# Kernel tuning notes

Measured on AMD Instinct MI355X. Metric: run time of the kernel, lower is better.

The kernel has to match this reference:

```python
import math
import jax, jax.numpy as jnp
import numpy as np

DIM = 2048
HID = 4 * DIM
SEQ = 2048
BATCH = 2
EPS = 1e-5


def _layernorm(x, g, b):
    mu = jnp.mean(x, axis=-1, keepdims=True)
    var = jnp.var(x, axis=-1, keepdims=True)
    return (x - mu) * jax.lax.rsqrt(var + EPS) * g + b


def setup_inputs() -> dict:
    key = jax.random.key(0)
    ks = jax.random.split(key, 12)
    s = 1.0 / math.sqrt(DIM)
    x = jax.random.normal(ks[0], (BATCH, SEQ, DIM), dtype=jnp.float32)
    # additive causal mask: 0 on/below diagonal, -1e9 above
    mask = jnp.where(jnp.tril(jnp.ones((SEQ, SEQ), dtype=bool)), 0.0, -1e9).astype(jnp.float32)
    freqs_cis = jax.random.normal(ks[1], (SEQ, 64), dtype=jnp.float32)  # unused by forward
    return {
        "x": x,
        "mask": mask,
        "start_pos": 0,
        "freqs_cis": freqs_cis,
        "wq": jax.random.normal(ks[2], (DIM, DIM), dtype=jnp.float32) * s,
        "bq": jnp.zeros((DIM,), dtype=jnp.float32),
        "wk": jax.random.normal(ks[3], (DIM, DIM), dtype=jnp.float32) * s,
        "bk": jnp.zeros((DIM,), dtype=jnp.float32),
        "wv": jax.random.normal(ks[4], (DIM, DIM), dtype=jnp.float32) * s,
        "bv": jnp.zeros((DIM,), dtype=jnp.float32),
        "g_ln1": jnp.ones((DIM,), dtype=jnp.float32),
        "b_ln1": jnp.zeros((DIM,), dtype=jnp.float32),
        "g_ln2": jnp.ones((DIM,), dtype=jnp.float32),
        "b_ln2": jnp.zeros((DIM,), dtype=jnp.float32),
        "w1": jax.random.normal(ks[5], (DIM, HID), dtype=jnp.float32) * s,
        "b1": jnp.zeros((HID,), dtype=jnp.float32),
        "w2": jax.random.normal(ks[6], (HID, DIM), dtype=jnp.float32) * (1.0 / math.sqrt(HID)),
        "b2": jnp.zeros((DIM,), dtype=jnp.float32),
    }


def reference(x, mask, start_pos, freqs_cis, wq, bq, wk, bk, wv, bv,
              g_ln1, b_ln1, g_ln2, b_ln2, w1, b1, w2, b2):
    # pre-norm attention (no head split; scale by sqrt(full dim); dropout=eval identity)
    h = _layernorm(x, g_ln1, b_ln1)
    q = h @ wq + bq
    k = h @ wk + bk
    v = h @ wv + bv
    scores = jnp.einsum('bqd,bkd->bqk', q, k) / math.sqrt(DIM) + mask
    attn = jax.nn.softmax(scores, axis=-1)
    attn_out = jnp.einsum('bqk,bkd->bqd', attn, v)
    h2 = _layernorm(x + attn_out, g_ln2, b_ln2)
    ffn = jax.nn.gelu(h2 @ w1 + b1, approximate=False) @ w2 + b2
    # NOTE: original code adds FFN output to the ORIGINAL x (attn residual dropped here)
    return x + ffn
```

## Files before the change

### kernel.cpp

```cpp
#include <hip/hip_runtime.h>
#include <math.h>

#define DIM_ 2048
#define HID_ 8192
#define SEQ_ 2048
#define BATCH_ 2
#define TOK_ (BATCH_*SEQ_)

typedef __attribute__((ext_vector_type(4))) float f32x4;
typedef __attribute__((ext_vector_type(8))) __bf16 bf16x8;
typedef __attribute__((ext_vector_type(4))) unsigned int u32x4;
typedef __attribute__((ext_vector_type(4))) short s16x4;
typedef __attribute__((ext_vector_type(8))) short s16x8;
typedef __attribute__((address_space(3))) short* lds_sp;

__device__ __forceinline__ short f2bf(float f) {
  union { float f; unsigned u; } v; v.f = f;
  unsigned r = v.u + 0x7FFFu + ((v.u >> 16) & 1u);
  return (short)(r >> 16);
}
__device__ __forceinline__ float bf2f(short s) {
  union { unsigned u; float f; } v; v.u = ((unsigned)(unsigned short)s) << 16;
  return v.f;
}

__device__ __forceinline__ f32x4 mfma16(u32x4 a, u32x4 b, f32x4 c) {
  return __builtin_amdgcn_mfma_f32_16x16x32_bf16(
      __builtin_bit_cast(bf16x8, a), __builtin_bit_cast(bf16x8, b), c, 0, 0, 0);
}

#define DSR(dst, addr) asm volatile("ds_read_b128 %0, %1" : "=v"(dst) : "v"(addr))
#define BARv()  __builtin_amdgcn_s_barrier()
#define LGKMW(n) do { asm volatile("s_waitcnt lgkmcnt(" #n ")" ::: "memory"); \
                      __builtin_amdgcn_sched_barrier(0); } while(0)
#define VM3()   asm volatile("s_waitcnt vmcnt(3)" ::: "memory")
#define VM4()   asm volatile("s_waitcnt vmcnt(4)" ::: "memory")
#define PRIO1() __builtin_amdgcn_s_setprio(1)
#define PRIO0() __builtin_amdgcn_s_setprio(0)

#define TILE_MAP(BM, BN) \
  const int nwg  = gridDim.x * gridDim.y; \
  const int orig = blockIdx.y * gridDim.x + blockIdx.x; \
  const int wgid = (orig & 7) * (nwg >> 3) + (orig >> 3); \
  const int gy4  = (int)gridDim.y << 2; \
  const int rem  = wgid % gy4; \
  const int tn   = ((wgid / gy4) * 4 + (rem & 3)) * (BN); \
  const int tm   = (rem >> 2) * (BM);

template<int EPI>
__device__ __forceinline__ void epi_store(void* Cv, const float* bias, const float* aux,
                                          int z, long long sC, int ldc, int N,
                                          int row, int col, float v)
{
  if (EPI == 1) {
    ((float*)Cv + (long long)z * sC)[(long long)row * ldc + col] = v;
  } else if (EPI == 0) {
    v += bias[col];
    ((short*)Cv + (long long)z * sC)[(long long)row * ldc + col] = f2bf(v);
  } else if (EPI == 2) {
    v += bias[col];
    v = 0.5f * v * (1.0f + erff(v * 0.70710678118654752f));
    ((short*)Cv + (long long)z * sC)[(long long)row * ldc + col] = f2bf(v);
  } else if (EPI == 3) {
    v += bias[col] + aux[(long long)row * ldc + col];
    ((float*)Cv + (long long)z * sC)[(long long)row * ldc + col] = v;
  } else {
    v = v * 0.022097086912079608f + aux[(long long)row * ldc + col];
    ((short*)Cv + (long long)z * sC)[(long long)row * ldc + col] = f2bf(v);
  }
}

#define G256_RD1(slot) do { \
  const unsigned s_ = (unsigned)(slot)*16384u; \
  DSR(af[0], aRd + s_);          DSR(af[1], aRd + s_ + 1024u); \
  DSR(af[2], aRd + s_ + 2048u);  DSR(af[3], aRd + s_ + 3072u); \
  DSR(af[4], aRd + s_ + 4096u);  DSR(af[5], aRd + s_ + 5120u); \
  DSR(af[6], aRd + s_ + 6144u);  DSR(af[7], aRd + s_ + 7168u); \
  DSR(bf0[0], bRd + s_);         DSR(bf0[1], bRd + s_ + 1024u); \
} while(0)

#define G256_RD2(slot) do { \
  const unsigned s_ = (unsigned)(slot)*16384u; \
  DSR(bf1[0], bRd + s_ + 2048u); DSR(bf1[1], bRd + s_ + 3072u); \
} while(0)

#define G256_MM(c0, bA, bB) do { \
  _Pragma("unroll") \
  for (int fr_ = 0; fr_ < 8; ++fr_) { \
    acc[fr_][(c0)]   = mfma16(af[fr_], bA, acc[fr_][(c0)]); \
    acc[fr_][(c0)+1] = mfma16(af[fr_], bB, acc[fr_][(c0)+1]); \
  } \
} while(0)

template<int EPI>
__global__ __launch_bounds__(512, 2)
void gemm256(const short* __restrict__ A, const short* __restrict__ B,
             void* __restrict__ Cv, const float* __restrict__ bias,
             const float* __restrict__ aux,
             int M, int N, int K, int lda, int ldb, int ldc,
             long long sA, long long sB, long long sC)
{
  __shared__ __align__(16) short As[3*256*32];
  __shared__ __align__(16) short Bs[3*256*32];
  const int lane = threadIdx.x & 63;
  const int wave = threadIdx.x >> 6;
  const int wr = wave >> 2, wc = wave & 3;
  TILE_MAP(256, 256)
  const int z = blockIdx.z;
  A += (long long)z * sA;
  B += (long long)z * sB;

  const int NT = K >> 5;

  const int rr   = wave * 16 + (lane >> 2);
  const int soff = (((lane & 3) ^ ((lane >> 3) & 3)) << 3);
  const short* pA = A + (long long)(tm + rr) * lda + soff;
  const short* pB = B + (long long)(tn + rr) * ldb + soff;
  const long long lda128 = 128LL * lda;
  const long long ldb128 = 128LL * ldb;

  auto stA = [&](int t, int slot) {
    const long long ko = (long long)t << 5;
    __builtin_amdgcn_global_load_lds(
        (const __attribute__((address_space(1))) void*)(pA + ko),
        (__attribute__((address_space(3))) void*)(As + slot * 8192 + wave * 512), 16, 0, 0);
    __builtin_amdgcn_global_load_lds(
        (const __attribute__((address_space(1))) void*)(pA + lda128 + ko),
        (__attribute__((address_space(3))) void*)(As + slot * 8192 + 4096 + wave * 512), 16, 0, 0);
  };
  auto stB = [&](int t, int slot) {
    const long long ko = (long long)t << 5;
    __builtin_amdgcn_global_load_lds(
        (const __attribute__((address_space(1))) void*)(pB + ko),
        (__attribute__((address_space(3))) void*)(Bs + slot * 8192 + wave * 512), 16, 0, 0);
    __builtin_amdgcn_global_load_lds(
        (const __attribute__((address_space(1))) void*)(pB + ldb128 + ko),
        (__attribute__((address_space(3))) void*)(Bs + slot * 8192 + 4096 + wave * 512), 16, 0, 0);
  };

  const unsigned asB = (unsigned)(unsigned long long)(lds_sp)As;
  const unsigned bsB = (unsigned)(unsigned long long)(lds_sp)Bs;
  const int l15 = lane & 15, l4 = lane >> 4;
  const unsigned offk = (unsigned)((l4 ^ ((l15 >> 1) & 3)) << 4);
  const unsigned aRd = asB + (unsigned)((wr * 128 + l15) * 64) + offk;
  const unsigned bRd = bsB + (unsigned)((wc * 64 + l15) * 64) + offk;

  f32x4 acc[8][4] = {};
  u32x4 af[8], bf0[2], bf1[2];

  stA(0, 0); stB(0, 0);
  stA(1 < NT ? 1 : 0, 1); stB(1 < NT ? 1 : 0, 1);
  VM4();
  BARv();

  int rd = 0;
  #pragma unroll 1
  for (int t = 0; t < NT; ++t) {
    const int st = rd + 2 >= 3 ? rd - 1 : rd + 2;
    const int tc = t + 2 < NT ? t + 2 : NT - 1;
    G256_RD1(rd);
    G256_RD2(rd);
    stA(tc, st); stB(tc, st);
    LGKMW(2);
    PRIO1(); G256_MM(0, bf0[0], bf0[1]);
    LGKMW(0);
    G256_MM(2, bf1[0], bf1[1]); PRIO0();
    VM4();
    BARv();
    rd = rd + 1 >= 3 ? 0 : rd + 1;
  }

  const int row0 = tm + wr * 128 + l4 * 4;
  const int col0 = tn + wc * 64 + l15;
  #pragma unroll
  for (int fr = 0; fr < 8; ++fr)
    #pragma unroll
    for (int j = 0; j < 4; ++j)
      #pragma unroll
      for (int fc = 0; fc < 4; ++fc)
        epi_store<EPI>(Cv, bias, aux, z, sC, ldc, N,
                       row0 + fr * 16 + j, col0 + fc * 16, acc[fr][fc][j]);
}

#define HRD2(slot) do { \
  const unsigned a_ = aBaseH + (unsigned)(slot)*8192u; \
  const unsigned b_ = bBaseH + (unsigned)(slot)*16384u; \
  DSR(bf[0], b_ + offk);          DSR(bf[1], b_ + 1024u + offk); \
  DSR(bf[2], b_ + 2048u + offk);  DSR(bf[3], b_ + 3072u + offk); \
  DSR(af[0], a_ + offk);          DSR(af[1], a_ + 1024u + offk); \
  DSR(af[2], a_ + 2048u + offk);  DSR(af[3], a_ + 3072u + offk); \
} while(0)

#define HROW(mi) do { \
  _Pragma("unroll") \
  for (int ni = 0; ni < 4; ++ni) \
    acc[mi][ni] = mfma16(af[mi], bf[ni], acc[mi][ni]); \
} while(0)

template<int EPI>
__global__ __launch_bounds__(512, 4)
void gemm_hi(const short* __restrict__ A, const short* __restrict__ B,
             void* __restrict__ Cv, const float* __restrict__ bias,
             const float* __restrict__ aux,
             int M, int N, int K, int lda, int ldb, int ldc,
             long long sA, long long sB, long long sC)
{
  __shared__ __align__(16) short As[3*128*32];
  __shared__ __align__(16) short Bs[3*256*32];
  const int lane = threadIdx.x & 63;
  const int wave = threadIdx.x >> 6;
  const int wr = wave >> 2, wc = wave & 3;
  TILE_MAP(128, 256)
  const int z = blockIdx.z;
  A += (long long)z * sA;
  B += (long long)z * sB;

  const int NT = K >> 5;

  const int rr   = wave * 16 + (lane >> 2);
  const int soff = (((lane & 3) ^ ((lane >> 3) & 3)) << 3);
  const short* pA = A + (long long)(tm + rr) * lda + soff;
  const short* pB = B + (long long)(tn + rr) * ldb + soff;
  const long long ldb128 = 128LL * ldb;

  auto stage = [&](int t, int slot) {
    const long long ko = (long long)t << 5;
    __builtin_amdgcn_global_load_lds(
        (const __attribute__((address_space(1))) void*)(pA + ko),
        (__attribute__((address_space(3))) void*)(As + slot * 4096 + wave * 512), 16, 0, 0);
    __builtin_amdgcn_global_load_lds(
        (const __attribute__((address_space(1))) void*)(pB + ko),
        (__attribute__((address_space(3))) void*)(Bs + slot * 8192 + wave * 512), 16, 0, 0);
    __builtin_amdgcn_global_load_lds(
        (const __attribute__((address_space(1))) void*)(pB + ldb128 + ko),
        (__attribute__((address_space(3))) void*)(Bs + slot * 8192 + 4096 + wave * 512), 16, 0, 0);
  };

  const unsigned asB = (unsigned)(unsigned long long)(lds_sp)As;
  const unsigned bsB = (unsigned)(unsigned long long)(lds_sp)Bs;
  const int l15 = lane & 15, l4 = lane >> 4;
  const unsigned offk  = (unsigned)((l4 ^ ((l15 >> 1) & 3)) << 4);
  const unsigned aBaseH = asB + (unsigned)(wr * 4096 + l15 * 64);
  const unsigned bBaseH = bsB + (unsigned)(wc * 4096 + l15 * 64);

  f32x4 acc[4][4] = {};
  u32x4 af[4], bf[4];

  stage(0, 0);
  stage(1 < NT ? 1 : 0, 1);
  VM3();
  BARv();

  int rd = 0;
  #pragma unroll 1
  for (int t = 0; t < NT; ++t) {
    const int st = rd + 2 >= 3 ? rd - 1 : rd + 2;
    const int tc = t + 2 < NT ? t + 2 : NT - 1;
    HRD2(rd);
    stage(tc, st);
    LGKMW(3);
    PRIO1(); HROW(0);
    LGKMW(2); HROW(1);
    LGKMW(1); HROW(2);
    LGKMW(0); HROW(3); PRIO0();
    VM3();
    BARv();
    rd = rd + 1 >= 3 ? 0 : rd + 1;
  }

  const int row0 = tm + wr * 64 + l4 * 4;
  const int col0 = tn + wc * 64 + l15;
  #pragma unroll
  for (int mi = 0; mi < 4; ++mi)
    #pragma unroll
    for (int j = 0; j < 4; ++j)
      #pragma unroll
      for (int ni = 0; ni < 4; ++ni)
        epi_store<EPI>(Cv, bias, aux, z, sC, ldc, N,
                       row0 + mi * 16 + j, col0 + ni * 16, acc[mi][ni][j]);
}

__global__ __launch_bounds__(256)
void ln_kernel(const float* __restrict__ x, const float* __restrict__ res,
               const float* __restrict__ g, const float* __restrict__ b,
               short* __restrict__ out, int hasres)
{
  const int row = blockIdx.x;
  const int tid = threadIdx.x;
  const float4* X = (const float4*)x + (long long)row * 512;
  float4 v0 = X[tid], v1 = X[tid + 256];
  if (hasres) {
    const float4* R = (const float4*)res + (long long)row * 512;
    float4 r0 = R[tid], r1 = R[tid + 256];
    v0.x += r0.x; v0.y += r0.y; v0.z += r0.z; v0.w += r0.w;
    v1.x += r1.x; v1.y += r1.y; v1.z += r1.z; v1.w += r1.w;
  }
  float s1 = v0.x + v0.y + v0.z + v0.w + v1.x + v1.y + v1.z + v1.w;
  float s2 = v0.x*v0.x + v0.y*v0.y + v0.z*v0.z + v0.w*v0.w
           + v1.x*v1.x + v1.y*v1.y + v1.z*v1.z + v1.w*v1.w;
  #pragma unroll
  for (int o = 32; o > 0; o >>= 1) { s1 += __shfl_xor(s1, o); s2 += __shfl_xor(s2, o); }
  __shared__ float red[8];
  if ((tid & 63) == 0) { red[tid >> 6] = s1; red[4 + (tid >> 6)] = s2; }
  __syncthreads();
  s1 = red[0] + red[1] + red[2] + red[3];
  s2 = red[4] + red[5] + red[6] + red[7];
  const float mean = s1 * (1.0f / 2048.0f);
  const float var  = s2 * (1.0f / 2048.0f) - mean * mean;
  const float rstd = rsqrtf(var + 1e-5f);
  const float4* G  = (const float4*)g;
  const float4* Bb = (const float4*)b;
  float4 g0 = G[tid], g1 = G[tid + 256], b0 = Bb[tid], b1 = Bb[tid + 256];
  s16x4 o0, o1;
  o0[0] = f2bf((v0.x - mean) * rstd * g0.x + b0.x);
  o0[1] = f2bf((v0.y - mean) * rstd * g0.y + b0.y);
  o0[2] = f2bf((v0.z - mean) * rstd * g0.z + b0.z);
  o0[3] = f2bf((v0.w - mean) * rstd * g0.w + b0.w);
  o1[0] = f2bf((v1.x - mean) * rstd * g1.x + b1.x);
  o1[1] = f2bf((v1.y - mean) * rstd * g1.y + b1.y);
  o1[2] = f2bf((v1.z - mean) * rstd * g1.z + b1.z);
  o1[3] = f2bf((v1.w - mean) * rstd * g1.w + b1.w);
  *(s16x4*)&out[(long long)row * 2048 + tid * 4]        = o0;
  *(s16x4*)&out[(long long)row * 2048 + 1024 + tid * 4] = o1;
}

__global__ __launch_bounds__(256)
void softmax_bf16_kernel(short* __restrict__ probs)
{
  const long long row = blockIdx.x;
  const int tid = threadIdx.x;
  short* P = probs + row * 2048 + tid * 8;
  s16x8 in = *(const s16x8*)P;
  float a[8];
  #pragma unroll
  for (int i = 0; i < 8; ++i) a[i] = bf2f(in[i]);
  float mx = a[0];
  #pragma unroll
  for (int i = 1; i < 8; ++i) mx = fmaxf(mx, a[i]);
  #pragma unroll
  for (int o = 32; o > 0; o >>= 1) mx = fmaxf(mx, __shfl_xor(mx, o));
  __shared__ float red[8];
  if ((tid & 63) == 0) red[tid >> 6] = mx;
  __syncthreads();
  mx = fmaxf(fmaxf(red[0], red[1]), fmaxf(red[2], red[3]));
  float e[8], sum = 0.f;
  #pragma unroll
  for (int i = 0; i < 8; ++i) { e[i] = __expf(a[i] - mx); sum += e[i]; }
  #pragma unroll
  for (int o = 32; o > 0; o >>= 1) sum += __shfl_xor(sum, o);
  if ((tid & 63) == 0) red[4 + (tid >> 6)] = sum;
  __syncthreads();
  sum = red[4] + red[5] + red[6] + red[7];
  const float inv = 1.0f / sum;
  s16x8 o;
  #pragma unroll
  for (int i = 0; i < 8; ++i) o[i] = f2bf(e[i] * inv);
  *(s16x8*)P = o;
}

__global__ __launch_bounds__(256)
void cvt_transpose64(const float* __restrict__ in, short* __restrict__ out,
                     int R, int C)
{
  __shared__ float t[64][69];
  const int r0 = blockIdx.y << 6, c0 = blockIdx.x << 6;
  const int tx = threadIdx.x & 15, ty = threadIdx.x >> 4;
  #pragma unroll
  for (int p = 0; p < 4; ++p) {
    const int r = ty + p * 16;
    float4 v = *(const float4*)&in[(long long)(r0 + r) * C + c0 + tx * 4];
    t[r][tx*4+0] = v.x; t[r][tx*4+1] = v.y; t[r][tx*4+2] = v.z; t[r][tx*4+3] = v.w;
  }
  __syncthreads();
  #pragma unroll
  for (int p = 0; p < 4; ++p) {
    const int oc = ty + p * 16;
    s16x4 o;
    o[0] = f2bf(t[tx*4+0][oc]); o[1] = f2bf(t[tx*4+1][oc]);
    o[2] = f2bf(t[tx*4+2][oc]); o[3] = f2bf(t[tx*4+3][oc]);
    *(s16x4*)&out[(long long)(c0 + oc) * R + r0 + tx * 4] = o;
  }
}

__global__ __launch_bounds__(256)
void transpose_bf16_kernel(const short* __restrict__ in, short* __restrict__ out,
                           int ldin, int ldout, long long sin_, long long sout_)
{
  __shared__ short t[32][33];
  in  += (long long)blockIdx.z * sin_;
  out += (long long)blockIdx.z * sout_;
  const int tx = threadIdx.x & 31, ty = threadIdx.x >> 5;
  const int r0 = blockIdx.y << 5, c0 = blockIdx.x << 5;
  #pragma unroll
  for (int i = 0; i < 32; i += 8)
    t[ty + i][tx] = in[(long long)(r0 + ty + i) * ldin + c0 + tx];
  __syncthreads();
  #pragma unroll
  for (int i = 0; i < 32; i += 8)
    out[(long long)(c0 + ty + i) * ldout + r0 + tx] = t[tx][ty + i];
}

__global__ __launch_bounds__(256)
void concat_bias_kernel(const float* a, const float* b, const float* c, float* o)
{
  const int i = blockIdx.x * 256 + threadIdx.x;
  o[i] = i < 2048 ? a[i] : (i < 4096 ? b[i - 2048] : c[i - 4096]);
}

extern "C" void kernel_launch(void* const* d_in, const int* in_sizes, int n_in,
                              void* d_out, int out_size, void* d_ws, size_t ws_size,
                              hipStream_t stream)
{
  const float* x    = (const float*)d_in[0];
  const float* mask = (const float*)d_in[1];
  const float* wq   = (const float*)d_in[4];
  const float* bq   = (const float*)d_in[5];
  const float* wk   = (const float*)d_in[6];
  const float* bk   = (const float*)d_in[7];
  const float* wv   = (const float*)d_in[8];
  const float* bv   = (const float*)d_in[9];
  const float* g1   = (const float*)d_in[10];
  const float* b1   = (const float*)d_in[11];
  const float* g2   = (const float*)d_in[12];
  const float* b2   = (const float*)d_in[13];
  const float* w1   = (const float*)d_in[14];
  const float* bw1  = (const float*)d_in[15];
  const float* w2   = (const float*)d_in[16];
  const float* bw2  = (const float*)d_in[17];
  float* out = (float*)d_out;

  char* p = (char*)d_ws;
  auto take = [&](size_t bytes) { char* r = p; p += (bytes + 255) & ~(size_t)255; return r; };
  short* wqkvT = (short*)take((size_t)3 * DIM_ * DIM_ * 2);
  short* w1T   = (short*)take((size_t)DIM_ * HID_ * 2);
  short* w2T   = (short*)take((size_t)HID_ * DIM_ * 2);
  short* h_bf  = (short*)take((size_t)TOK_ * DIM_ * 2);
  short* qkv   = (short*)take((size_t)TOK_ * 3 * DIM_ * 2);
  short* vT    = (short*)take((size_t)BATCH_ * DIM_ * SEQ_ * 2);
  float* attno = (float*)take((size_t)TOK_ * DIM_ * 4);
  short* attn  = (short*)take((size_t)BATCH_ * SEQ_ * SEQ_ * 2);
  float* cbias = (float*)take((size_t)3 * DIM_ * 4);
  short* ffn1  = qkv;
  short* h2    = h_bf;

  const dim3 blk(256), gblk(512);
  cvt_transpose64<<<dim3(DIM_/64, DIM_/64), blk, 0, stream>>>(wq, wqkvT, DIM_, DIM_);
  cvt_transpose64<<<dim3(DIM_/64, DIM_/64), blk, 0, stream>>>(wk, wqkvT + (size_t)DIM_*DIM_, DIM_, DIM_);
  cvt_transpose64<<<dim3(DIM_/64, DIM_/64), blk, 0, stream>>>(wv, wqkvT + (size_t)2*DIM_*DIM_, DIM_, DIM_);
  cvt_transpose64<<<dim3(HID_/64, DIM_/64), blk, 0, stream>>>(w1, w1T, DIM_, HID_);
  cvt_transpose64<<<dim3(DIM_/64, HID_/64), blk, 0, stream>>>(w2, w2T, HID_, DIM_);
  concat_bias_kernel<<<24, blk, 0, stream>>>(bq, bk, bv, cbias);
  ln_kernel<<<TOK_, blk, 0, stream>>>(x, nullptr, g1, b1, h_bf, 0);
  gemm256<0><<<dim3(6144/256, TOK_/256, 1), gblk, 0, stream>>>(
      h_bf, wqkvT, qkv, cbias, nullptr, TOK_, 6144, DIM_, DIM_, DIM_, 6144, 0, 0, 0);
  gemm_hi<4><<<dim3(SEQ_/256, SEQ_/128, BATCH_), gblk, 0, stream>>>(
      qkv, qkv + DIM_, attn, nullptr, mask, SEQ_, SEQ_, DIM_, 6144, 6144, SEQ_,
      (long long)SEQ_ * 6144, (long long)SEQ_ * 6144, (long long)SEQ_ * SEQ_);
  softmax_bf16_kernel<<<BATCH_ * SEQ_, blk, 0, stream>>>(attn);
  transpose_bf16_kernel<<<dim3(DIM_/32, SEQ_/32, BATCH_), blk, 0, stream>>>(
      qkv + 2*DIM_, vT, 6144, SEQ_, (long long)SEQ_ * 6144, (long long)DIM_ * SEQ_);
  gemm_hi<1><<<dim3(DIM_/256, SEQ_/128, BATCH_), gblk, 0, stream>>>(
      attn, vT, attno, nullptr, nullptr, SEQ_, DIM_, SEQ_, SEQ_, SEQ_, DIM_,
      (long long)SEQ_ * SEQ_, (long long)DIM_ * SEQ_, (long long)SEQ_ * DIM_);
  ln_kernel<<<TOK_, blk, 0, stream>>>(x, attno, g2, b2, h2, 1);
  gemm256<2><<<dim3(HID_/256, TOK_/256, 1), gblk, 0, stream>>>(
      h2, w1T, ffn1, bw1, nullptr, TOK_, HID_, DIM_, DIM_, DIM_, HID_, 0, 0, 0);
  gemm_hi<3><<<dim3(DIM_/256, TOK_/128, 1), gblk, 0, stream>>>(
      ffn1, w2T, out, bw2, x, TOK_, DIM_, HID_, HID_, HID_, DIM_, 0, 0, 0);
}
```

Measured before the change: 625.2 us.

## Replace 256x256 GEMM main loop with 8-phase ping-pong schedule using K=64 tiles

```diff
diff --git a/kernel.cpp b/kernel.cpp
--- a/kernel.cpp
+++ b/kernel.cpp
@@ -37,6 +37,8 @@
 #define VM4()   asm volatile("s_waitcnt vmcnt(4)" ::: "memory")
 #define PRIO1() __builtin_amdgcn_s_setprio(1)
 #define PRIO0() __builtin_amdgcn_s_setprio(0)
+#define AS1 const __attribute__((address_space(1))) void*
+#define AS3 __attribute__((address_space(3))) void*
 
 #define TILE_MAP(BM, BN) \
   const int nwg  = gridDim.x * gridDim.y; \
@@ -70,38 +72,43 @@
   }
 }
 
-#define G256_RD1(slot) do { \
-  const unsigned s_ = (unsigned)(slot)*16384u; \
-  DSR(af[0], aRd + s_);          DSR(af[1], aRd + s_ + 1024u); \
-  DSR(af[2], aRd + s_ + 2048u);  DSR(af[3], aRd + s_ + 3072u); \
-  DSR(af[4], aRd + s_ + 4096u);  DSR(af[5], aRd + s_ + 5120u); \
-  DSR(af[6], aRd + s_ + 6144u);  DSR(af[7], aRd + s_ + 7168u); \
-  DSR(bf0[0], bRd + s_);         DSR(bf0[1], bRd + s_ + 1024u); \
-} while(0)
-
-#define G256_RD2(slot) do { \
-  const unsigned s_ = (unsigned)(slot)*16384u; \
-  DSR(bf1[0], bRd + s_ + 2048u); DSR(bf1[1], bRd + s_ + 3072u); \
-} while(0)
-
-#define G256_MM(c0, bA, bB) do { \
+#define RD_A4(frb, bo) do { \
   _Pragma("unroll") \
-  for (int fr_ = 0; fr_ < 8; ++fr_) { \
-    acc[fr_][(c0)]   = mfma16(af[fr_], bA, acc[fr_][(c0)]); \
-    acc[fr_][(c0)+1] = mfma16(af[fr_], bB, acc[fr_][(c0)+1]); \
+  for (int fr_ = 0; fr_ < 4; ++fr_) { \
+    DSR(af[fr_][0], aBase + (bo) + ((frb) + fr_) * 2048u + offk0); \
+    DSR(af[fr_][1], aBase + (bo) + ((frb) + fr_) * 2048u + offk1); \
   } \
 } while(0)
 
+#define RD_B2(fcb, bo) do { \
+  _Pragma("unroll") \
+  for (int i_ = 0; i_ < 2; ++i_) { \
+    DSR(bfr[(fcb) + i_][0], bBase + (bo) + ((fcb) + i_) * 2048u + offk0); \
+    DSR(bfr[(fcb) + i_][1], bBase + (bo) + ((fcb) + i_) * 2048u + offk1); \
+  } \
+} while(0)
+
+#define MM16(frb, fcb) do { \
+  _Pragma("unroll") \
+  for (int fr_ = 0; fr_ < 4; ++fr_) { \
+    _Pragma("unroll") \
+    for (int c_ = 0; c_ < 2; ++c_) { \
+      acc[(frb)+fr_][(fcb)+c_] = mfma16(af[fr_][0], bfr[(fcb)+c_][0], acc[(frb)+fr_][(fcb)+c_]); \
+      acc[(frb)+fr_][(fcb)+c_] = mfma16(af[fr_][1], bfr[(fcb)+c_][1], acc[(frb)+fr_][(fcb)+c_]); \
+    } \
+  } \
+} while(0)
+
 template<int EPI>
 __global__ __launch_bounds__(512, 2)
-void gemm256(const short* __restrict__ A, const short* __restrict__ B,
+void gemm8ph(const short* __restrict__ A, const short* __restrict__ B,
              void* __restrict__ Cv, const float* __restrict__ bias,
              const float* __restrict__ aux,
              int M, int N, int K, int lda, int ldb, int ldc,
              long long sA, long long sB, long long sC)
 {
-  __shared__ __align__(16) short As[3*256*32];
-  __shared__ __align__(16) short Bs[3*256*32];
+  __shared__ __align__(16) short As[2*2*128*64];
+  __shared__ __align__(16) short Bs[2*2*128*64];
   const int lane = threadIdx.x & 63;
   const int wave = threadIdx.x >> 6;
   const int wr = wave >> 2, wc = wave & 3;
@@ -110,64 +117,110 @@
   A += (long long)z * sA;
   B += (long long)z * sB;
 
-  const int NT = K >> 5;
-
-  const int rr   = wave * 16 + (lane >> 2);
-  const int soff = (((lane & 3) ^ ((lane >> 3) & 3)) << 3);
-  const short* pA = A + (long long)(tm + rr) * lda + soff;
-  const short* pB = B + (long long)(tn + rr) * ldb + soff;
-  const long long lda128 = 128LL * lda;
-  const long long ldb128 = 128LL * ldb;
-
-  auto stA = [&](int t, int slot) {
-    const long long ko = (long long)t << 5;
-    __builtin_amdgcn_global_load_lds(
-        (const __attribute__((address_space(1))) void*)(pA + ko),
-        (__attribute__((address_space(3))) void*)(As + slot * 8192 + wave * 512), 16, 0, 0);
-    __builtin_amdgcn_global_load_lds(
-        (const __attribute__((address_space(1))) void*)(pA + lda128 + ko),
-        (__attribute__((address_space(3))) void*)(As + slot * 8192 + 4096 + wave * 512), 16, 0, 0);
+  const int NT = K >> 6;
+  const int NI = NT >> 1;
+
+  const int srow = wave * 8 + (lane >> 3);
+  const int soff = (((lane & 7) ^ ((wave * 4 + (lane >> 4)) & 7)) << 3);
+  const short* pA = A + (long long)(tm + srow) * lda + soff;
+  const short* pB = B + (long long)(tn + srow) * ldb + soff;
+
+  auto stA = [&](int tt, int b, int h) {
+    const short* s = pA + (long long)(h * 128) * lda + ((long long)tt << 6);
+    __builtin_amdgcn_global_load_lds((AS1)s,
+        (AS3)(As + b * 16384 + h * 8192 + wave * 512), 16, 0, 0);
+    __builtin_amdgcn_global_load_lds((AS1)(s + 64LL * lda),
+        (AS3)(As + b * 16384 + h * 8192 + 4096 + wave * 512), 16, 0, 0);
   };
-  auto stB = [&](int t, int slot) {
-    const long long ko = (long long)t << 5;
-    __builtin_amdgcn_global_load_lds(
-        (const __attribute__((address_space(1))) void*)(pB + ko),
-        (__attribute__((address_space(3))) void*)(Bs + slot * 8192 + wave * 512), 16, 0, 0);
-    __builtin_amdgcn_global_load_lds(
-        (const __attribute__((address_space(1))) void*)(pB + ldb128 + ko),
-        (__attribute__((address_space(3))) void*)(Bs + slot * 8192 + 4096 + wave * 512), 16, 0, 0);
+  auto stB = [&](int tt, int b, int h) {
+    const short* s = pB + (long long)(h * 128) * ldb + ((long long)tt << 6);
+    __builtin_amdgcn_global_load_lds((AS1)s,
+        (AS3)(Bs + b * 16384 + h * 8192 + wave * 512), 16, 0, 0);
+    __builtin_amdgcn_global_load_lds((AS1)(s + 64LL * ldb),
+        (AS3)(Bs + b * 16384 + h * 8192 + 4096 + wave * 512), 16, 0, 0);
   };
 
   const unsigned asB = (unsigned)(unsigned long long)(lds_sp)As;
   const unsigned bsB = (unsigned)(unsigned long long)(lds_sp)Bs;
   const int l15 = lane & 15, l4 = lane >> 4;
-  const unsigned offk = (unsigned)((l4 ^ ((l15 >> 1) & 3)) << 4);
-  const unsigned aRd = asB + (unsigned)((wr * 128 + l15) * 64) + offk;
-  const unsigned bRd = bsB + (unsigned)((wc * 64 + l15) * 64) + offk;
+  const unsigned fswz = (unsigned)((l15 >> 1) & 7);
+  const unsigned offk0 = (((unsigned)l4 ^ fswz) << 4);
+  const unsigned offk1 = ((((unsigned)l4 + 4u) ^ fswz) << 4);
+  const unsigned aBase = asB + (unsigned)(wr * 16384 + l15 * 128);
+  const unsigned bBase = bsB + (unsigned)((wc >> 1) * 16384 + (wc & 1) * 8192 + l15 * 128);
 
   f32x4 acc[8][4] = {};
-  u32x4 af[8], bf0[2], bf1[2];
-
-  stA(0, 0); stB(0, 0);
-  stA(1 < NT ? 1 : 0, 1); stB(1 < NT ? 1 : 0, 1);
+  u32x4 af[4][2], bfr[4][2];
+
+  stA(0, 0, 0); stA(0, 0, 1); stB(0, 0, 0); stB(0, 0, 1);
+  stB(1, 1, 0); stB(1, 1, 1);
   VM4();
   BARv();
 
-  int rd = 0;
   #pragma unroll 1
-  for (int t = 0; t < NT; ++t) {
-    const int st = rd + 2 >= 3 ? rd - 1 : rd + 2;
-    const int tc = t + 2 < NT ? t + 2 : NT - 1;
-    G256_RD1(rd);
-    G256_RD2(rd);
-    stA(tc, st); stB(tc, st);
-    LGKMW(2);
-    PRIO1(); G256_MM(0, bf0[0], bf0[1]);
-    LGKMW(0);
-    G256_MM(2, bf1[0], bf1[1]); PRIO0();
-    VM4();
-    BARv();
-    rd = rd + 1 >= 3 ? 0 : rd + 1;
+  for (int i = 0; i < NI; ++i) {
+    const int t1c = 2 * i + 1;
+    const int t2  = (2 * i + 2 < NT) ? 2 * i + 2 : NT - 1;
+    const int t3  = (2 * i + 3 < NT) ? 2 * i + 3 : NT - 1;
+
+    {
+      RD_A4(0, 0u); RD_B2(0, 0u);
+      stA(t1c, 1, 0);
+      LGKMW(8);
+      BARv(); LGKMW(0);
+      PRIO1(); MM16(0, 0); PRIO0();
+      BARv();
+    }
+    {
+      RD_B2(2, 0u);
+      stA(t1c, 1, 1);
+      BARv(); LGKMW(0);
+      PRIO1(); MM16(0, 2); PRIO0();
+      BARv();
+    }
+    {
+      RD_A4(4, 0u);
+      stB(t2, 0, 0);
+      BARv(); LGKMW(0);
+      PRIO1(); MM16(4, 0); PRIO0();
+      BARv();
+    }
+    {
+      stB(t2, 0, 1);
+      VM4();
+      BARv();
+      PRIO1(); MM16(4, 2); PRIO0();
+      BARv();
+    }
+    {
+      RD_A4(0, 32768u); RD_B2(0, 32768u);
+      stA(t2, 0, 0);
+      LGKMW(8);
+      BARv(); LGKMW(0);
+      PRIO1(); MM16(0, 0); PRIO0();
+      BARv();
+    }
+    {
+      RD_B2(2, 32768u);
+      stA(t2, 0, 1);
+      BARv(); LGKMW(0);
+      PRIO1(); MM16(0, 2); PRIO0();
+      BARv();
+    }
+    {
+      RD_A4(4, 32768u);
+      stB(t3, 1, 0);
+      BARv(); LGKMW(0);
+      PRIO1(); MM16(4, 0); PRIO0();
+      BARv();
+    }
+    {
+      stB(t3, 1, 1);
+      VM4();
+      BARv();
+      PRIO1(); MM16(4, 2); PRIO0();
+      BARv();
+    }
   }
 
   const int row0 = tm + wr * 128 + l4 * 4;
@@ -225,15 +278,12 @@
 
   auto stage = [&](int t, int slot) {
     const long long ko = (long long)t << 5;
-    __builtin_amdgcn_global_load_lds(
-        (const __attribute__((address_space(1))) void*)(pA + ko),
-        (__attribute__((address_space(3))) void*)(As + slot * 4096 + wave * 512), 16, 0, 0);
-    __builtin_amdgcn_global_load_lds(
-        (const __attribute__((address_space(1))) void*)(pB + ko),
-        (__attribute__((address_space(3))) void*)(Bs + slot * 8192 + wave * 512), 16, 0, 0);
-    __builtin_amdgcn_global_load_lds(
-        (const __attribute__((address_space(1))) void*)(pB + ldb128 + ko),
-        (__attribute__((address_space(3))) void*)(Bs + slot * 8192 + 4096 + wave * 512), 16, 0, 0);
+    __builtin_amdgcn_global_load_lds((AS1)(pA + ko),
+        (AS3)(As + slot * 4096 + wave * 512), 16, 0, 0);
+    __builtin_amdgcn_global_load_lds((AS1)(pB + ko),
+        (AS3)(Bs + slot * 8192 + wave * 512), 16, 0, 0);
+    __builtin_amdgcn_global_load_lds((AS1)(pB + ldb128 + ko),
+        (AS3)(Bs + slot * 8192 + 4096 + wave * 512), 16, 0, 0);
   };
 
   const unsigned asB = (unsigned)(unsigned long long)(lds_sp)As;
@@ -451,7 +501,7 @@
   cvt_transpose64<<<dim3(DIM_/64, HID_/64), blk, 0, stream>>>(w2, w2T, HID_, DIM_);
   concat_bias_kernel<<<24, blk, 0, stream>>>(bq, bk, bv, cbias);
   ln_kernel<<<TOK_, blk, 0, stream>>>(x, nullptr, g1, b1, h_bf, 0);
-  gemm256<0><<<dim3(6144/256, TOK_/256, 1), gblk, 0, stream>>>(
+  gemm8ph<0><<<dim3(6144/256, TOK_/256, 1), gblk, 0, stream>>>(
       h_bf, wqkvT, qkv, cbias, nullptr, TOK_, 6144, DIM_, DIM_, DIM_, 6144, 0, 0, 0);
   gemm_hi<4><<<dim3(SEQ_/256, SEQ_/128, BATCH_), gblk, 0, stream>>>(
       qkv, qkv + DIM_, attn, nullptr, mask, SEQ_, SEQ_, DIM_, 6144, 6144, SEQ_,
@@ -463,7 +513,7 @@
       attn, vT, attno, nullptr, nullptr, SEQ_, DIM_, SEQ_, SEQ_, SEQ_, DIM_,
       (long long)SEQ_ * SEQ_, (long long)DIM_ * SEQ_, (long long)SEQ_ * DIM_);
   ln_kernel<<<TOK_, blk, 0, stream>>>(x, attno, g2, b2, h2, 1);
-  gemm256<2><<<dim3(HID_/256, TOK_/256, 1), gblk, 0, stream>>>(
+  gemm8ph<2><<<dim3(HID_/256, TOK_/256, 1), gblk, 0, stream>>>(
       h2, w1T, ffn1, bw1, nullptr, TOK_, HID_, DIM_, DIM_, DIM_, HID_, 0, 0, 0);
   gemm_hi<3><<<dim3(DIM_/256, TOK_/128, 1), gblk, 0, stream>>>(
       ffn1, w2T, out, bw2, x, TOK_, DIM_, HID_, HID_, HID_, DIM_, 0, 0, 0);
```

New measurement: 674.6 us. 1.08x slower.

## Replace pipelined GEMM kernels with simple single-buffered 128x128 tile kernel

Applied to the files above, without the earlier changes.

```diff
diff --git a/kernel.cpp b/kernel.cpp
--- a/kernel.cpp
+++ b/kernel.cpp
@@ -28,15 +28,19 @@
   return __builtin_amdgcn_mfma_f32_16x16x32_bf16(
       __builtin_bit_cast(bf16x8, a), __builtin_bit_cast(bf16x8, b), c, 0, 0, 0);
 }
+__device__ __forceinline__ f32x4 mfma16v(bf16x8 a, bf16x8 b, f32x4 c) {
+  return __builtin_amdgcn_mfma_f32_16x16x32_bf16(a, b, c, 0, 0, 0);
+}
 
 #define DSR(dst, addr) asm volatile("ds_read_b128 %0, %1" : "=v"(dst) : "v"(addr))
 #define BARv()  __builtin_amdgcn_s_barrier()
 #define LGKMW(n) do { asm volatile("s_waitcnt lgkmcnt(" #n ")" ::: "memory"); \
                       __builtin_amdgcn_sched_barrier(0); } while(0)
-#define VM3()   asm volatile("s_waitcnt vmcnt(3)" ::: "memory")
 #define VM4()   asm volatile("s_waitcnt vmcnt(4)" ::: "memory")
 #define PRIO1() __builtin_amdgcn_s_setprio(1)
 #define PRIO0() __builtin_amdgcn_s_setprio(0)
+#define AS1 const __attribute__((address_space(1))) void*
+#define AS3 __attribute__((address_space(3))) void*
 
 #define TILE_MAP(BM, BN) \
   const int nwg  = gridDim.x * gridDim.y; \
@@ -70,6 +74,77 @@
   }
 }
 
+template<int EPI>
+__global__ __launch_bounds__(256, 3)
+void gemm97(const short* __restrict__ A, const short* __restrict__ B,
+            void* __restrict__ Cv, const float* __restrict__ bias,
+            const float* __restrict__ aux,
+            int M, int N, int K, int lda, int ldb, int ldc,
+            long long sA, long long sB, long long sC)
+{
+  __shared__ __align__(16) short As[128*32];
+  __shared__ __align__(16) short Bs[128*32];
+  const int lane = threadIdx.x & 63;
+  const int wave = threadIdx.x >> 6;
+  const int wr = wave >> 1, wc = wave & 1;
+  TILE_MAP(128, 128)
+  const int z = blockIdx.z;
+  A += (long long)z * sA;
+  B += (long long)z * sB;
+
+  const int NT = K >> 5;
+
+  const int srow = wave * 16 + (lane >> 2);
+  const int soff = (((lane & 3) ^ ((lane >> 3) & 3)) << 3);
+  const short* pA = A + (long long)(tm + srow) * lda + soff;
+  const short* pB = B + (long long)(tn + srow) * ldb + soff;
+  const long long lda64 = 64LL * lda;
+  const long long ldb64 = 64LL * ldb;
+
+  const int l15 = lane & 15, l4 = lane >> 4;
+  const int koff = ((l4 ^ ((l15 >> 1) & 3)) << 3);
+  const int arow = wr * 64 + l15;
+  const int brow = wc * 64 + l15;
+
+  f32x4 acc[4][4] = {};
+
+  #pragma unroll 1
+  for (int t = 0; t < NT; ++t) {
+    const long long ko = (long long)t << 5;
+    __builtin_amdgcn_global_load_lds((AS1)(pA + ko),
+        (AS3)(As + wave * 512), 16, 0, 0);
+    __builtin_amdgcn_global_load_lds((AS1)(pA + lda64 + ko),
+        (AS3)(As + 2048 + wave * 512), 16, 0, 0);
+    __builtin_amdgcn_global_load_lds((AS1)(pB + ko),
+        (AS3)(Bs + wave * 512), 16, 0, 0);
+    __builtin_amdgcn_global_load_lds((AS1)(pB + ldb64 + ko),
+        (AS3)(Bs + 2048 + wave * 512), 16, 0, 0);
+    __syncthreads();
+    bf16x8 af[4], bfr[4];
+    #pragma unroll
+    for (int i = 0; i < 4; ++i) af[i]  = *(const bf16x8*)&As[(arow + i * 16) * 32 + koff];
+    #pragma unroll
+    for (int i = 0; i < 4; ++i) bfr[i] = *(const bf16x8*)&Bs[(brow + i * 16) * 32 + koff];
+    #pragma unroll
+    for (int mi = 0; mi < 4; ++mi)
+      #pragma unroll
+      for (int ni = 0; ni < 4; ++ni)
+        acc[mi][ni] = mfma16v(af[mi], bfr[ni], acc[mi][ni]);
+    __syncthreads();
+  }
+
+  const int row0 = tm + wr * 64 + l4 * 4;
+  const int col0 = tn + wc * 64 + l15;
+  #pragma unroll
+  for (int mi = 0; mi < 4; ++mi)
+    #pragma unroll
+    for (int j = 0; j < 4; ++j)
+      #pragma unroll
+      for (int ni = 0; ni < 4; ++ni)
+        epi_store<EPI>(Cv, bias, aux, z, sC, ldc, N,
+                       row0 + mi * 16 + j, col0 + ni * 16, acc[mi][ni][j]);
+}
+
 #define G256_RD1(slot) do { \
   const unsigned s_ = (unsigned)(slot)*16384u; \
   DSR(af[0], aRd + s_);          DSR(af[1], aRd + s_ + 1024u); \
@@ -121,21 +196,17 @@
 
   auto stA = [&](int t, int slot) {
     const long long ko = (long long)t << 5;
-    __builtin_amdgcn_global_load_lds(
-        (const __attribute__((address_space(1))) void*)(pA + ko),
-        (__attribute__((address_space(3))) void*)(As + slot * 8192 + wave * 512), 16, 0, 0);
-    __builtin_amdgcn_global_load_lds(
-        (const __attribute__((address_space(1))) void*)(pA + lda128 + ko),
-        (__attribute__((address_space(3))) void*)(As + slot * 8192 + 4096 + wave * 512), 16, 0, 0);
+    __builtin_amdgcn_global_load_lds((AS1)(pA + ko),
+        (AS3)(As + slot * 8192 + wave * 512), 16, 0, 0);
+    __builtin_amdgcn_global_load_lds((AS1)(pA + lda128 + ko),
+        (AS3)(As + slot * 8192 + 4096 + wave * 512), 16, 0, 0);
   };
   auto stB = [&](int t, int slot) {
     const long long ko = (long long)t << 5;
-    __builtin_amdgcn_global_load_lds(
-        (const __attribute__((address_space(1))) void*)(pB + ko),
-        (__attribute__((address_space(3))) void*)(Bs + slot * 8192 + wave * 512), 16, 0, 0);
-    __builtin_amdgcn_global_load_lds(
-        (const __attribute__((address_space(1))) void*)(pB + ldb128 + ko),
-        (__attribute__((address_space(3))) void*)(Bs + slot * 8192 + 4096 + wave * 512), 16, 0, 0);
+    __builtin_amdgcn_global_load_lds((AS1)(pB + ko),
+        (AS3)(Bs + slot * 8192 + wave * 512), 16, 0, 0);
+    __builtin_amdgcn_global_load_lds((AS1)(pB + ldb128 + ko),
+        (AS3)(Bs + slot * 8192 + 4096 + wave * 512), 16, 0, 0);
   };
 
   const unsigned asB = (unsigned)(unsigned long long)(lds_sp)As;
@@ -180,104 +251,6 @@
       for (int fc = 0; fc < 4; ++fc)
         epi_store<EPI>(Cv, bias, aux, z, sC, ldc, N,
                        row0 + fr * 16 + j, col0 + fc * 16, acc[fr][fc][j]);
-}
-
-#define HRD2(slot) do { \
-  const unsigned a_ = aBaseH + (unsigned)(slot)*8192u; \
-  const unsigned b_ = bBaseH + (unsigned)(slot)*16384u; \
-  DSR(bf[0], b_ + offk);          DSR(bf[1], b_ + 1024u + offk); \
-  DSR(bf[2], b_ + 2048u + offk);  DSR(bf[3], b_ + 3072u + offk); \
-  DSR(af[0], a_ + offk);          DSR(af[1], a_ + 1024u + offk); \
-  DSR(af[2], a_ + 2048u + offk);  DSR(af[3], a_ + 3072u + offk); \
-} while(0)
-
-#define HROW(mi) do { \
-  _Pragma("unroll") \
-  for (int ni = 0; ni < 4; ++ni) \
-    acc[mi][ni] = mfma16(af[mi], bf[ni], acc[mi][ni]); \
-} while(0)
-
-template<int EPI>
-__global__ __launch_bounds__(512, 4)
-void gemm_hi(const short* __restrict__ A, const short* __restrict__ B,
-             void* __restrict__ Cv, const float* __restrict__ bias,
-             const float* __restrict__ aux,
-             int M, int N, int K, int lda, int ldb, int ldc,
-             long long sA, long long sB, long long sC)
-{
-  __shared__ __align__(16) short As[3*128*32];
-  __shared__ __align__(16) short Bs[3*256*32];
-  const int lane = threadIdx.x & 63;
-  const int wave = threadIdx.x >> 6;
-  const int wr = wave >> 2, wc = wave & 3;
-  TILE_MAP(128, 256)
-  const int z = blockIdx.z;
-  A += (long long)z * sA;
-  B += (long long)z * sB;
-
-  const int NT = K >> 5;
-
-  const int rr   = wave * 16 + (lane >> 2);
-  const int soff = (((lane & 3) ^ ((lane >> 3) & 3)) << 3);
-  const short* pA = A + (long long)(tm + rr) * lda + soff;
-  const short* pB = B + (long long)(tn + rr) * ldb + soff;
-  const long long ldb128 = 128LL * ldb;
-
-  auto stage = [&](int t, int slot) {
-    const long long ko = (long long)t << 5;
-    __builtin_amdgcn_global_load_lds(
-        (const __attribute__((address_space(1))) void*)(pA + ko),
-        (__attribute__((address_space(3))) void*)(As + slot * 4096 + wave * 512), 16, 0, 0);
-    __builtin_amdgcn_global_load_lds(
-        (const __attribute__((address_space(1))) void*)(pB + ko),
-        (__attribute__((address_space(3))) void*)(Bs + slot * 8192 + wave * 512), 16, 0, 0);
-    __builtin_amdgcn_global_load_lds(
-        (const __attribute__((address_space(1))) void*)(pB + ldb128 + ko),
-        (__attribute__((address_space(3))) void*)(Bs + slot * 8192 + 4096 + wave * 512), 16, 0, 0);
-  };
-
-  const unsigned asB = (unsigned)(unsigned long long)(lds_sp)As;
-  const unsigned bsB = (unsigned)(unsigned long long)(lds_sp)Bs;
-  const int l15 = lane & 15, l4 = lane >> 4;
-  const unsigned offk  = (unsigned)((l4 ^ ((l15 >> 1) & 3)) << 4);
-  const unsigned aBaseH = asB + (unsigned)(wr * 4096 + l15 * 64);
-  const unsigned bBaseH = bsB + (unsigned)(wc * 4096 + l15 * 64);
-
-  f32x4 acc[4][4] = {};
-  u32x4 af[4], bf[4];
-
-  stage(0, 0);
-  stage(1 < NT ? 1 : 0, 1);
-  VM3();
-  BARv();
-
-  int rd = 0;
-  #pragma unroll 1
-  for (int t = 0; t < NT; ++t) {
-    const int st = rd + 2 >= 3 ? rd - 1 : rd + 2;
-    const int tc = t + 2 < NT ? t + 2 : NT - 1;
-    HRD2(rd);
-    stage(tc, st);
-    LGKMW(3);
-    PRIO1(); HROW(0);
-    LGKMW(2); HROW(1);
-    LGKMW(1); HROW(2);
-    LGKMW(0); HROW(3); PRIO0();
-    VM3();
-    BARv();
-    rd = rd + 1 >= 3 ? 0 : rd + 1;
-  }
-
-  const int row0 = tm + wr * 64 + l4 * 4;
-  const int col0 = tn + wc * 64 + l15;
-  #pragma unroll
-  for (int mi = 0; mi < 4; ++mi)
-    #pragma unroll
-    for (int j = 0; j < 4; ++j)
-      #pragma unroll
-      for (int ni = 0; ni < 4; ++ni)
-        epi_store<EPI>(Cv, bias, aux, z, sC, ldc, N,
-                       row0 + mi * 16 + j, col0 + ni * 16, acc[mi][ni][j]);
 }
 
 __global__ __launch_bounds__(256)
@@ -451,20 +424,20 @@
   cvt_transpose64<<<dim3(DIM_/64, HID_/64), blk, 0, stream>>>(w2, w2T, HID_, DIM_);
   concat_bias_kernel<<<24, blk, 0, stream>>>(bq, bk, bv, cbias);
   ln_kernel<<<TOK_, blk, 0, stream>>>(x, nullptr, g1, b1, h_bf, 0);
-  gemm256<0><<<dim3(6144/256, TOK_/256, 1), gblk, 0, stream>>>(
+  gemm97<0><<<dim3(6144/128, TOK_/128, 1), blk, 0, stream>>>(
       h_bf, wqkvT, qkv, cbias, nullptr, TOK_, 6144, DIM_, DIM_, DIM_, 6144, 0, 0, 0);
-  gemm_hi<4><<<dim3(SEQ_/256, SEQ_/128, BATCH_), gblk, 0, stream>>>(
+  gemm97<4><<<dim3(SEQ_/128, SEQ_/128, BATCH_), blk, 0, stream>>>(
       qkv, qkv + DIM_, attn, nullptr, mask, SEQ_, SEQ_, DIM_, 6144, 6144, SEQ_,
       (long long)SEQ_ * 6144, (long long)SEQ_ * 6144, (long long)SEQ_ * SEQ_);
   softmax_bf16_kernel<<<BATCH_ * SEQ_, blk, 0, stream>>>(attn);
   transpose_bf16_kernel<<<dim3(DIM_/32, SEQ_/32, BATCH_), blk, 0, stream>>>(
       qkv + 2*DIM_, vT, 6144, SEQ_, (long long)SEQ_ * 6144, (long long)DIM_ * SEQ_);
-  gemm_hi<1><<<dim3(DIM_/256, SEQ_/128, BATCH_), gblk, 0, stream>>>(
+  gemm97<1><<<dim3(DIM_/128, SEQ_/128, BATCH_), blk, 0, stream>>>(
       attn, vT, attno, nullptr, nullptr, SEQ_, DIM_, SEQ_, SEQ_, SEQ_, DIM_,
       (long long)SEQ_ * SEQ_, (long long)DIM_ * SEQ_, (long long)SEQ_ * DIM_);
   ln_kernel<<<TOK_, blk, 0, stream>>>(x, attno, g2, b2, h2, 1);
   gemm256<2><<<dim3(HID_/256, TOK_/256, 1), gblk, 0, stream>>>(
       h2, w1T, ffn1, bw1, nullptr, TOK_, HID_, DIM_, DIM_, DIM_, HID_, 0, 0, 0);
-  gemm_hi<3><<<dim3(DIM_/256, TOK_/128, 1), gblk, 0, stream>>>(
+  gemm97<3><<<dim3(DIM_/128, TOK_/128, 1), blk, 0, stream>>>(
       ffn1, w2T, out, bw2, x, TOK_, DIM_, HID_, HID_, HID_, DIM_, 0, 0, 0);
 }
```

After: 692.7 us. 1.11x slower.
